# Performance work log

Hardware: AMD Instinct MI355X
Metric: run time of the kernel (lower is better)

Reference implementation:

```python
import jax, jax.numpy as jnp
import numpy as np

HALF = 16  # num_outputs // 2 with num_features = 32
EPS = 1e-5


def _gmul(Wm, h):
    # Wm: [B,N,M,J], h: [B,M,F] -> [B,N,J*F] (j-major feature layout, matching torch split/cat/bmm)
    B, N = Wm.shape[0], Wm.shape[1]
    return jnp.einsum('bnmj,bmf->bnjf', Wm, h).reshape(B, N, -1)


def _bn(z, g, b):
    # training-mode BatchNorm2d on [R, C, 1, 1] == per-channel norm over rows, biased var
    m = z.mean(axis=0)
    v = z.var(axis=0)
    return g * (z - m) / jnp.sqrt(v + EPS) + b


def _block(W, hx, W_lg, hy, P, wx2x, wy2x, bx, wy2y, wx2y, by, gx, btx, gy, bty):
    B, N, M = P.shape[0], P.shape[1], P.shape[2]
    x2x = _gmul(W, hx).reshape(-1, wx2x.shape[0])
    y2x = _gmul(P, hy).reshape(-1, wy2x.shape[0])
    zx = x2x @ wx2x + y2x @ wy2x + bx
    zx = jnp.concatenate([jax.nn.relu(zx[:, :HALF]), zx[:, HALF:]], axis=1)
    xo = _bn(zx, gx, btx).reshape(B, N, -1)
    y2y = _gmul(W_lg, hy).reshape(-1, wy2y.shape[0])
    x2y = _gmul(jnp.swapaxes(P, 1, 2), hx).reshape(-1, wx2y.shape[0])
    zy = y2y @ wy2y + x2y @ wx2y + by
    zy = jnp.concatenate([jax.nn.relu(zy[:, :HALF]), zy[:, HALF:]], axis=1)
    yo = _bn(zy, gy, bty).reshape(B, M, -1)
    return xo, yo


def _forward(W, x, W_lg, y, P,
             wx2x0, wy2x0, bx0, wy2y0, wx2y0, by0, gx0, btx0, gy0, bty0,
             wx2x_m, wy2x_m, bx_m, wy2y_m, wx2y_m, by_m, gx_m, btx_m, gy_m, bty_m,
             wlx, wly, bl):
    hx, hy = _block(W, x, W_lg, y, P, wx2x0, wy2x0, bx0, wy2y0, wx2y0, by0,
                    gx0, btx0, gy0, bty0)
    for i in range(wx2x_m.shape[0]):  # fixed num_layers loop
        hx, hy = _block(W, hx, W_lg, hy, P,
                        wx2x_m[i], wy2x_m[i], bx_m[i], wy2y_m[i], wx2y_m[i], by_m[i],
                        gx_m[i], btx_m[i], gy_m[i], bty_m[i])
    # final layer: linear only, x branch output
    x2x = _gmul(W, hx).reshape(-1, wlx.shape[0])
    y2x = _gmul(P, hy).reshape(-1, wly.shape[0])
    out = (x2x @ wlx + y2x @ wly + bl).reshape(W.shape[0], W.shape[1], -1)
    return out


def setup_inputs() -> dict:
    key = jax.random.key(0)
    ks = iter(jax.random.split(key, 40))
    B, N, M, J, F, L, C = 1, 2048, 4096, 3, 32, 6, 2
    d = {}
    d['W'] = jax.random.normal(next(ks), (B, N, N, J), jnp.float32)
    d['x'] = jax.random.normal(next(ks), (B, N, 1), jnp.float32)
    d['W_lg'] = jax.random.normal(next(ks), (B, M, M, J), jnp.float32)
    d['y'] = jax.random.normal(next(ks), (B, M, 1), jnp.float32)
    d['P'] = jax.random.normal(next(ks), (B, N, M, 2), jnp.float32)
    s = 0.1
    d['wx2x0'] = jax.random.normal(next(ks), (J * 1, F), jnp.float32) * s
    d['wy2x0'] = jax.random.normal(next(ks), (2 * 1, F), jnp.float32) * s
    d['bx0'] = jax.random.normal(next(ks), (F,), jnp.float32) * s
    d['wy2y0'] = jax.random.normal(next(ks), (J * 1, F), jnp.float32) * s
    d['wx2y0'] = jax.random.normal(next(ks), (2 * 1, F), jnp.float32) * s
    d['by0'] = jax.random.normal(next(ks), (F,), jnp.float32) * s
    d['gx0'] = jnp.ones((F,), jnp.float32)
    d['btx0'] = jnp.zeros((F,), jnp.float32)
    d['gy0'] = jnp.ones((F,), jnp.float32)
    d['bty0'] = jnp.zeros((F,), jnp.float32)
    d['wx2x_m'] = jax.random.normal(next(ks), (L, J * F, F), jnp.float32) * s
    d['wy2x_m'] = jax.random.normal(next(ks), (L, 2 * F, F), jnp.float32) * s
    d['bx_m'] = jax.random.normal(next(ks), (L, F), jnp.float32) * s
    d['wy2y_m'] = jax.random.normal(next(ks), (L, J * F, F), jnp.float32) * s
    d['wx2y_m'] = jax.random.normal(next(ks), (L, 2 * F, F), jnp.float32) * s
    d['by_m'] = jax.random.normal(next(ks), (L, F), jnp.float32) * s
    d['gx_m'] = jnp.ones((L, F), jnp.float32)
    d['btx_m'] = jnp.zeros((L, F), jnp.float32)
    d['gy_m'] = jnp.ones((L, F), jnp.float32)
    d['bty_m'] = jnp.zeros((L, F), jnp.float32)
    d['wlx'] = jax.random.normal(next(ks), (J * F, C), jnp.float32) * s
    d['wly'] = jax.random.normal(next(ks), (2 * F, C), jnp.float32) * s
    d['bl'] = jax.random.normal(next(ks), (C,), jnp.float32) * s
    return d


def reference(W, x, W_lg, y, P,
              wx2x0, wy2x0, bx0, wy2y0, wx2y0, by0, gx0, btx0, gy0, bty0,
              wx2x_m, wy2x_m, bx_m, wy2y_m, wx2y_m, by_m, gx_m, btx_m, gy_m, bty_m,
              wlx, wly, bl):
    return _forward(W, x, W_lg, y, P,
                    wx2x0, wy2x0, bx0, wy2y0, wx2y0, by0, gx0, btx0, gy0, bty0,
                    wx2x_m, wy2x_m, bx_m, wy2y_m, wx2y_m, by_m, gx_m, btx_m, gy_m, bty_m,
                    wlx, wly, bl)
```

## Files before the change

kernel.cpp:

```cpp
#include <hip/hip_runtime.h>

typedef _Float16 f16x8 __attribute__((ext_vector_type(8)));
typedef float f32x4 __attribute__((ext_vector_type(4)));


__device__ inline unsigned short f16b(float v) {
    _Float16 h = (_Float16)v;
    return __builtin_bit_cast(unsigned short, h);
}

__device__ inline void atomAddF(float* p, float v) {
    __hip_atomic_fetch_add(p, v, __ATOMIC_RELAXED, __HIP_MEMORY_SCOPE_AGENT);
}

template<int K>
__device__ inline void pack_cvt(const float* __restrict__ src, unsigned short* __restrict__ dst, int u) {
    int o = u * 8;
    int panel = o / (K * 16);
    int rem = o - panel * (K * 16);
    int kstep = rem >> 9;
    int rem2 = rem & 511;
    int g = rem2 >> 7;
    int r15 = (rem2 >> 3) & 15;
    int row = (panel << 4) | r15;
    int k = (kstep << 5) | (g << 3);
    const float4* s = (const float4*)(src + (size_t)row * K + k);
    float4 v0 = s[0], v1 = s[1];
    uint4 q;
    q.x = (unsigned)f16b(v0.x) | ((unsigned)f16b(v0.y) << 16);
    q.y = (unsigned)f16b(v0.z) | ((unsigned)f16b(v0.w) << 16);
    q.z = (unsigned)f16b(v1.x) | ((unsigned)f16b(v1.y) << 16);
    q.w = (unsigned)f16b(v1.z) | ((unsigned)f16b(v1.w) << 16);
    ((uint4*)dst)[u] = q;
}

__global__ __launch_bounds__(256) void cvt_pack(const float* __restrict__ W, const float* __restrict__ WL,
                                                unsigned short* __restrict__ Wb, unsigned short* __restrict__ WLb) {
    const int NW = 1572864, TOT = 1572864 + 6291456;
    for (int u = blockIdx.x * 256 + threadIdx.x; u < TOT; u += 2048 * 256) {
        if (u < NW) pack_cvt<6144>(W, Wb, u);
        else pack_cvt<12288>(WL, WLb, u - NW);
    }
}

__global__ __launch_bounds__(256) void transpose_p(const float* __restrict__ P,
                                                   unsigned short* __restrict__ Pb,
                                                   unsigned short* __restrict__ PT) {
    __shared__ unsigned int lds[64][33];
    int bid = blockIdx.x;
    int m0 = (bid & 127) * 32;
    int n0 = (bid >> 7) * 64;
    int tid = threadIdx.x;
    const float2* P2 = (const float2*)P;
    #pragma unroll
    for (int it = 0; it < 8; ++it) {
        int idx = it * 256 + tid;
        int nl = idx >> 5, ml = idx & 31;
        float2 v = P2[(size_t)(n0 + nl) * 4096 + (m0 + ml)];
        unsigned int pk = (unsigned int)f16b(v.x) | ((unsigned int)f16b(v.y) << 16);
        lds[nl][ml] = pk;
    }
    __syncthreads();
    unsigned int* PTu = (unsigned int*)PT;
    #pragma unroll
    for (int it = 0; it < 8; ++it) {
        int idx = it * 256 + tid;
        int ml = idx >> 6, nl = idx & 63;
        int row = m0 + ml;
        int k2 = (n0 + nl) * 2;
        int o = ((row >> 4) << 16) | ((k2 >> 5) << 9) | (((((k2 >> 3) & 3) << 4) | (row & 15)) << 3) | (k2 & 7);
        PTu[o >> 1] = lds[nl][ml];
    }
    unsigned int* Pbu = (unsigned int*)Pb;
    #pragma unroll
    for (int it = 0; it < 8; ++it) {
        int idx = it * 256 + tid;
        int nl = idx >> 5, ml = idx & 31;
        int row = n0 + nl;
        int k = (m0 + ml) * 2;
        int o = (row >> 4) * 131072 + ((k >> 5) << 9) + (((((k >> 3) & 3) << 4) | (row & 15)) << 3) + (k & 7);
        Pbu[o >> 1] = lds[nl][ml];
    }
}

__global__ __launch_bounds__(256) void build_b(
    const float* __restrict__ srcx, const float* __restrict__ srcy,
    int Fin, int Fout, int buildB2, int use_bn,
    const float* __restrict__ stats,
    const float* __restrict__ w1a, const float* __restrict__ w1b,
    const float* __restrict__ w2a, const float* __restrict__ w2b,
    unsigned short* __restrict__ B1f, unsigned short* __restrict__ B2f) {
    int tid0 = blockIdx.x * 256 + threadIdx.x;
    const int NB1 = 14336 * 32;
    int isB2 = 0, t2 = tid0;
    if (tid0 >= NB1) {
        if (!buildB2) return;
        isB2 = 1; t2 = tid0 - NB1;
        if (t2 >= 16384 * 32) return;
    }
    int e = t2 & 7, lane = (t2 >> 3) & 63, hh = (t2 >> 9) & 1, t = t2 >> 10;
    int k = (t << 5) | ((lane >> 4) << 3) | e;
    int g = (hh << 4) | (lane & 15);
    float v = 0.f;
    if (g < Fout) {
        const float* hr; const float* wc; int useY;
        if (!isB2) {
            if (k < 6144) { int m = k / 3, j = k - 3 * m; hr = srcx + m * Fin; wc = w1a + (j * Fin) * Fout + g; useY = 0; }
            else { int k2 = k - 6144; int m = k2 >> 1, p = k2 & 1; hr = srcy + m * Fin; wc = w1b + (p * Fin) * Fout + g; useY = 1; }
        } else {
            if (k < 12288) { int m = k / 3, j = k - 3 * m; hr = srcy + m * Fin; wc = w2a + (j * Fin) * Fout + g; useY = 1; }
            else { int k2 = k - 12288; int n = k2 >> 1, p = k2 & 1; hr = srcx + n * Fin; wc = w2b + (p * Fin) * Fout + g; useY = 0; }
        }
        float a = 0.f;
        if (use_bn) {
            const float* sc = useY ? stats + 196 : stats + 132;
            const float* sh = useY ? stats + 228 : stats + 164;
            #pragma unroll
            for (int f = 0; f < 32; ++f) {
                float h = sc[f] * hr[f] + sh[f];
                a += h * wc[f * Fout];
            }
        } else {
            for (int f = 0; f < Fin; ++f) a += hr[f] * wc[f * Fout];
        }
        v = a;
    }
    if (!isB2) B1f[t2] = f16b(v); else B2f[t2] = f16b(v);
}

__global__ __launch_bounds__(256) void gemm_k(
    const unsigned short* __restrict__ Wb, const unsigned short* __restrict__ Pb,
    const unsigned short* __restrict__ WLb, const unsigned short* __restrict__ PTb,
    const unsigned short* __restrict__ B1f, const unsigned short* __restrict__ B2f,
    float* __restrict__ px, float* __restrict__ py, float* __restrict__ stats, int nwgx) {
    __shared__ float lds[4][1024];
    int bid = blockIdx.x;
    if (bid == 0 && threadIdx.x < 132) stats[threadIdx.x] = 0.f;
    const unsigned short* Bf;
    float* Z;
    int seg, Mbase, K, kloc, kb;
    const unsigned short* A16;
    if (bid < nwgx) {
        Bf = B1f;
        int mwg = bid / 14; seg = bid % 14;
        Mbase = mwg * 32;
        kb = seg << 10;
        Z = px + (size_t)seg * 65536;
        if (seg < 6) { K = 6144; kloc = kb;        A16 = Wb; }
        else         { K = 8192; kloc = kb - 6144; A16 = Pb; }
    } else {
        int b2 = bid - nwgx;
        Bf = B2f;
        int mwg = b2 / 16; seg = b2 % 16;
        Mbase = mwg * 32;
        kb = seg << 10;
        Z = py + (size_t)seg * 131072;
        if (seg < 12) { K = 12288; kloc = kb;         A16 = WLb; }
        else          { K = 4096;  kloc = kb - 12288; A16 = PTb; }
    }
    int wid = threadIdx.x >> 6, lane = threadIdx.x & 63;
    int kq = wid << 8;
    const unsigned short* ap0 = A16 + (size_t)(Mbase >> 4) * (K * 16)
                              + (size_t)((kloc + kq) >> 5) * 512 + lane * 8;
    const unsigned short* ap1 = ap0 + (size_t)K * 16;
    const unsigned short* bp = Bf + ((size_t)((kb + kq) >> 5)) * 1024 + lane * 8;
    f32x4 acc00 = {0.f,0.f,0.f,0.f}, acc01 = {0.f,0.f,0.f,0.f};
    f32x4 acc10 = {0.f,0.f,0.f,0.f}, acc11 = {0.f,0.f,0.f,0.f};
    #pragma unroll
    for (int ks = 0; ks < 8; ++ks) {
        f16x8 a0 = *(const f16x8*)ap0;
        f16x8 a1 = *(const f16x8*)ap1;
        f16x8 b0 = *(const f16x8*)bp;
        f16x8 b1 = *(const f16x8*)(bp + 512);
        acc00 = __builtin_amdgcn_mfma_f32_16x16x32_f16(a0, b0, acc00, 0, 0, 0);
        acc10 = __builtin_amdgcn_mfma_f32_16x16x32_f16(a1, b0, acc10, 0, 0, 0);
        acc01 = __builtin_amdgcn_mfma_f32_16x16x32_f16(a0, b1, acc01, 0, 0, 0);
        acc11 = __builtin_amdgcn_mfma_f32_16x16x32_f16(a1, b1, acc11, 0, 0, 0);
        ap0 += 512; ap1 += 512; bp += 1024;
    }
    int col = lane & 15, r0 = (lane >> 4) << 2;
    float* l = lds[wid];
    #pragma unroll
    for (int r = 0; r < 4; ++r) {
        l[(r0 + r) * 32 + col]            = acc00[r];
        l[(r0 + r) * 32 + col + 16]       = acc01[r];
        l[(r0 + r + 16) * 32 + col]       = acc10[r];
        l[(r0 + r + 16) * 32 + col + 16]  = acc11[r];
    }
    __syncthreads();
    int t = threadIdx.x;
    float4 a = ((const float4*)lds[0])[t];
    float4 b = ((const float4*)lds[1])[t];
    float4 c = ((const float4*)lds[2])[t];
    float4 d = ((const float4*)lds[3])[t];
    float4 s;
    s.x = (a.x + b.x) + (c.x + d.x);
    s.y = (a.y + b.y) + (c.y + d.y);
    s.z = (a.z + b.z) + (c.z + d.z);
    s.w = (a.w + b.w) + (c.w + d.w);
    ((float4*)(Z + (size_t)Mbase * 32))[t] = s;
}

__global__ __launch_bounds__(256) void reduce_stats(
    const float* __restrict__ px, const float* __restrict__ py,
    const float* __restrict__ bx, const float* __restrict__ by,
    const float* __restrict__ gx, const float* __restrict__ btx,
    const float* __restrict__ gy, const float* __restrict__ bty,
    float* __restrict__ zax, float* __restrict__ zay,
    float* __restrict__ stats) {
    __shared__ float lsum[4][8][8];
    __shared__ int lastFlag;
    int bid = blockIdx.x, tid = threadIdx.x;
    const float4* src; const float* bias; float4* dst; float* st; int nseg, i4, stride4;
    if (bid < 64) { src = (const float4*)px; bias = bx; dst = (float4*)zax; st = stats;      nseg = 14; i4 = bid * 256 + tid;        stride4 = 16384; }
    else          { src = (const float4*)py; bias = by; dst = (float4*)zay; st = stats + 64; nseg = 16; i4 = (bid - 64) * 256 + tid; stride4 = 32768; }
    float4 s = {0.f, 0.f, 0.f, 0.f};
    for (int g = 0; g < nseg; ++g) {
        float4 v = src[(size_t)g * stride4 + i4];
        s.x += v.x; s.y += v.y; s.z += v.z; s.w += v.w;
    }
    int c0 = (i4 & 7) * 4;
    float4 b4 = *(const float4*)(bias + c0);
    s.x += b4.x; s.y += b4.y; s.z += b4.z; s.w += b4.w;
    if (c0 < 16) {
        s.x = fmaxf(s.x, 0.f); s.y = fmaxf(s.y, 0.f);
        s.z = fmaxf(s.z, 0.f); s.w = fmaxf(s.w, 0.f);
    }
    dst[i4] = s;
    float4 s2 = {s.x * s.x, s.y * s.y, s.z * s.z, s.w * s.w};
    #pragma unroll
    for (int mask = 8; mask <= 32; mask <<= 1) {
        s.x += __shfl_xor(s.x, mask); s.y += __shfl_xor(s.y, mask);
        s.z += __shfl_xor(s.z, mask); s.w += __shfl_xor(s.w, mask);
        s2.x += __shfl_xor(s2.x, mask); s2.y += __shfl_xor(s2.y, mask);
        s2.z += __shfl_xor(s2.z, mask); s2.w += __shfl_xor(s2.w, mask);
    }
    int w = tid >> 6, ln = tid & 63;
    if (ln < 8) {
        lsum[w][ln][0] = s.x;  lsum[w][ln][1] = s.y;  lsum[w][ln][2] = s.z;  lsum[w][ln][3] = s.w;
        lsum[w][ln][4] = s2.x; lsum[w][ln][5] = s2.y; lsum[w][ln][6] = s2.z; lsum[w][ln][7] = s2.w;
    }
    __syncthreads();
    if (tid < 64) {
        int q = tid >> 3, e = tid & 7;
        float v = lsum[0][q][e] + lsum[1][q][e] + lsum[2][q][e] + lsum[3][q][e];
        int col = q * 4 + (e & 3);
        atomAddF((e < 4) ? &st[col] : &st[32 + col], v);
    }
    __syncthreads();
    if (tid == 0) {
        __threadfence();
        int old = __hip_atomic_fetch_add((int*)(stats + 128), 1, __ATOMIC_ACQ_REL, __HIP_MEMORY_SCOPE_AGENT);
        lastFlag = (old == 191) ? 1 : 0;
    }
    __syncthreads();
    if (lastFlag && tid < 64) {
        int f = tid & 31, isY = tid >> 5;
        float* sb = stats + (isY ? 64 : 0);
        float n = isY ? 4096.f : 2048.f;
        float sum = __hip_atomic_load(&sb[f], __ATOMIC_RELAXED, __HIP_MEMORY_SCOPE_AGENT);
        float ssq = __hip_atomic_load(&sb[32 + f], __ATOMIC_RELAXED, __HIP_MEMORY_SCOPE_AGENT);
        float mean = sum / n;
        float var = ssq / n - mean * mean;
        const float* gv = isY ? gy : gx;
        const float* bv = isY ? bty : btx;
        float sc = gv[f] * rsqrtf(var + 1e-5f);
        stats[132 + isY * 64 + f] = sc;
        stats[164 + isY * 64 + f] = bv[f] - mean * sc;
    }
}

__global__ __launch_bounds__(256) void out_final(const float* __restrict__ px,
                                                 const float* __restrict__ bl,
                                                 float* __restrict__ out) {
    int tid = blockIdx.x * 256 + threadIdx.x;
    if (tid < 4096) {
        int n = tid >> 1, c = tid & 1;
        float a = bl[c];
        for (int s = 0; s < 14; ++s) a += px[(size_t)s * 65536 + n * 32 + c];
        out[tid] = a;
    }
}

extern "C" void kernel_launch(void* const* d_in, const int* in_sizes, int n_in,
                              void* d_out, int out_size, void* d_ws, size_t ws_size,
                              hipStream_t stream) {
    const float* W    = (const float*)d_in[0];
    const float* x    = (const float*)d_in[1];
    const float* WL   = (const float*)d_in[2];
    const float* y    = (const float*)d_in[3];
    const float* P    = (const float*)d_in[4];
    const float* wx2x0 = (const float*)d_in[5];
    const float* wy2x0 = (const float*)d_in[6];
    const float* bx0   = (const float*)d_in[7];
    const float* wy2y0 = (const float*)d_in[8];
    const float* wx2y0 = (const float*)d_in[9];
    const float* by0   = (const float*)d_in[10];
    const float* gx0   = (const float*)d_in[11];
    const float* btx0  = (const float*)d_in[12];
    const float* gy0   = (const float*)d_in[13];
    const float* bty0  = (const float*)d_in[14];
    const float* wx2x_m = (const float*)d_in[15];
    const float* wy2x_m = (const float*)d_in[16];
    const float* bx_m   = (const float*)d_in[17];
    const float* wy2y_m = (const float*)d_in[18];
    const float* wx2y_m = (const float*)d_in[19];
    const float* by_m   = (const float*)d_in[20];
    const float* gx_m   = (const float*)d_in[21];
    const float* btx_m  = (const float*)d_in[22];
    const float* gy_m   = (const float*)d_in[23];
    const float* bty_m  = (const float*)d_in[24];
    const float* wlx = (const float*)d_in[25];
    const float* wly = (const float*)d_in[26];
    const float* bl  = (const float*)d_in[27];

    char* base = (char*)d_ws;
    unsigned short* Wb  = (unsigned short*)(base + 0);
    unsigned short* Pb  = (unsigned short*)(base + 25165824);
    unsigned short* WLb = (unsigned short*)(base + 58720256);
    unsigned short* PTb = (unsigned short*)(base + 159383552);
    unsigned short* B1f = (unsigned short*)(base + 192937984);
    unsigned short* B2f = (unsigned short*)(base + 193855488);
    float* zax   = (float*)(base + 194904064);
    float* zay   = (float*)(base + 195166208);
    float* stats = (float*)(base + 195690496);
    float* px    = (float*)(base + 195692544);
    float* py    = (float*)(base + 199362560);

    cvt_pack<<<2048, 256, 0, stream>>>(W, WL, Wb, WLb);
    transpose_p<<<4096, 256, 0, stream>>>(P, Pb, PTb);

    build_b<<<3840, 256, 0, stream>>>(x, y, 1, 32, 1, 0, stats,
                                      wx2x0, wy2x0, wy2y0, wx2y0, B1f, B2f);
    gemm_k<<<2944, 256, 0, stream>>>(Wb, Pb, WLb, PTb, B1f, B2f, px, py, stats, 896);
    reduce_stats<<<192, 256, 0, stream>>>(px, py, bx0, by0, gx0, btx0, gy0, bty0, zax, zay, stats);

    for (int i = 0; i < 6; ++i) {
        build_b<<<3840, 256, 0, stream>>>(zax, zay, 32, 32, 1, 1, stats,
                                          wx2x_m + i * 3072, wy2x_m + i * 2048,
                                          wy2y_m + i * 3072, wx2y_m + i * 2048, B1f, B2f);
        gemm_k<<<2944, 256, 0, stream>>>(Wb, Pb, WLb, PTb, B1f, B2f, px, py, stats, 896);
        reduce_stats<<<192, 256, 0, stream>>>(px, py, bx_m + i * 32, by_m + i * 32,
                                              gx_m + i * 32, btx_m + i * 32,
                                              gy_m + i * 32, bty_m + i * 32, zax, zay, stats);
    }

    build_b<<<1792, 256, 0, stream>>>(zax, zay, 32, 2, 0, 1, stats,
                                      wlx, wly, nullptr, nullptr, B1f, B2f);
    gemm_k<<<896, 256, 0, stream>>>(Wb, Pb, WLb, PTb, B1f, B2f, px, py, stats, 896);
    out_final<<<16, 256, 0, stream>>>(px, bl, (float*)d_out);
}
```

Baseline: 679.7 us.

## Merge pack and transpose into one prep kernel; coalesce conversion reads

Fuses the fp16 pack/convert of W and W_lg with the P transpose into a single launch, with block ranges split between the two jobs. Each pack thread now reads a contiguous 32-float run of one row instead of 8 floats, and scatters four 16-byte stores. build_b is remapped so that adjacent threads share a k and differ in output column g, which makes the input-row reads broadcast-friendly while the stores become scattered. The intent is to cut launch overhead and improve read coalescing, at the cost of less regular writes.

```diff
diff --git a/kernel.cpp b/kernel.cpp
--- a/kernel.cpp
+++ b/kernel.cpp
@@ -14,42 +14,44 @@
 }
 
 template<int K>
-__device__ inline void pack_cvt(const float* __restrict__ src, unsigned short* __restrict__ dst, int u) {
-    int o = u * 8;
-    int panel = o / (K * 16);
-    int rem = o - panel * (K * 16);
-    int kstep = rem >> 9;
-    int rem2 = rem & 511;
-    int g = rem2 >> 7;
-    int r15 = (rem2 >> 3) & 15;
+__device__ inline void pack_cvt4(const float* __restrict__ src, unsigned short* __restrict__ dst, int q) {
+    const int KSTEPS = K / 32;
+    int r15 = q & 15;
+    int blk = q >> 4;
+    int panel = blk / KSTEPS;
+    int kstep = blk - panel * KSTEPS;
     int row = (panel << 4) | r15;
-    int k = (kstep << 5) | (g << 3);
-    const float4* s = (const float4*)(src + (size_t)row * K + k);
-    float4 v0 = s[0], v1 = s[1];
-    uint4 q;
-    q.x = (unsigned)f16b(v0.x) | ((unsigned)f16b(v0.y) << 16);
-    q.y = (unsigned)f16b(v0.z) | ((unsigned)f16b(v0.w) << 16);
-    q.z = (unsigned)f16b(v1.x) | ((unsigned)f16b(v1.y) << 16);
-    q.w = (unsigned)f16b(v1.z) | ((unsigned)f16b(v1.w) << 16);
-    ((uint4*)dst)[u] = q;
-}
-
-__global__ __launch_bounds__(256) void cvt_pack(const float* __restrict__ W, const float* __restrict__ WL,
-                                                unsigned short* __restrict__ Wb, unsigned short* __restrict__ WLb) {
-    const int NW = 1572864, TOT = 1572864 + 6291456;
-    for (int u = blockIdx.x * 256 + threadIdx.x; u < TOT; u += 2048 * 256) {
-        if (u < NW) pack_cvt<6144>(W, Wb, u);
-        else pack_cvt<12288>(WL, WLb, u - NW);
-    }
-}
-
-__global__ __launch_bounds__(256) void transpose_p(const float* __restrict__ P,
-                                                   unsigned short* __restrict__ Pb,
-                                                   unsigned short* __restrict__ PT) {
+    const float4* s = (const float4*)(src + (size_t)row * K + (kstep << 5));
+    uint4* d = (uint4*)dst;
+    #pragma unroll
+    for (int g = 0; g < 4; ++g) {
+        float4 v0 = s[g * 2], v1 = s[g * 2 + 1];
+        uint4 qq;
+        qq.x = (unsigned)f16b(v0.x) | ((unsigned)f16b(v0.y) << 16);
+        qq.y = (unsigned)f16b(v0.z) | ((unsigned)f16b(v0.w) << 16);
+        qq.z = (unsigned)f16b(v1.x) | ((unsigned)f16b(v1.y) << 16);
+        qq.w = (unsigned)f16b(v1.z) | ((unsigned)f16b(v1.w) << 16);
+        d[(size_t)blk * 64 + g * 16 + r15] = qq;
+    }
+}
+
+__global__ __launch_bounds__(256) void prep(const float* __restrict__ W, const float* __restrict__ WL,
+                                            const float* __restrict__ P,
+                                            unsigned short* __restrict__ Wb, unsigned short* __restrict__ WLb,
+                                            unsigned short* __restrict__ Pb, unsigned short* __restrict__ PT) {
     __shared__ unsigned int lds[64][33];
     int bid = blockIdx.x;
-    int m0 = (bid & 127) * 32;
-    int n0 = (bid >> 7) * 64;
+    if (bid < 2048) {
+        const int QW = 393216, QTOT = 393216 + 1572864;
+        for (int q = bid * 256 + threadIdx.x; q < QTOT; q += 2048 * 256) {
+            if (q < QW) pack_cvt4<6144>(W, Wb, q);
+            else pack_cvt4<12288>(WL, WLb, q - QW);
+        }
+        return;
+    }
+    int vb = bid - 2048;
+    int m0 = (vb & 127) * 32;
+    int n0 = (vb >> 7) * 64;
     int tid = threadIdx.x;
     const float2* P2 = (const float2*)P;
     #pragma unroll
@@ -90,17 +92,16 @@
     const float* __restrict__ w1a, const float* __restrict__ w1b,
     const float* __restrict__ w2a, const float* __restrict__ w2b,
     unsigned short* __restrict__ B1f, unsigned short* __restrict__ B2f) {
-    int tid0 = blockIdx.x * 256 + threadIdx.x;
+    int t2 = blockIdx.x * 256 + threadIdx.x;
     const int NB1 = 14336 * 32;
-    int isB2 = 0, t2 = tid0;
-    if (tid0 >= NB1) {
+    int isB2 = 0;
+    if (t2 >= NB1) {
         if (!buildB2) return;
-        isB2 = 1; t2 = tid0 - NB1;
+        isB2 = 1; t2 -= NB1;
         if (t2 >= 16384 * 32) return;
     }
-    int e = t2 & 7, lane = (t2 >> 3) & 63, hh = (t2 >> 9) & 1, t = t2 >> 10;
-    int k = (t << 5) | ((lane >> 4) << 3) | e;
-    int g = (hh << 4) | (lane & 15);
+    int g = t2 & 31;
+    int k = t2 >> 5;
     float v = 0.f;
     if (g < Fout) {
         const float* hr; const float* wc; int useY;
@@ -125,7 +126,9 @@
         }
         v = a;
     }
-    if (!isB2) B1f[t2] = f16b(v); else B2f[t2] = f16b(v);
+    int e = k & 7, kw = (k >> 3) & 3, t = k >> 5, hh = g >> 4;
+    int off = (((t * 2 + hh) * 64 + (kw << 4) + (g & 15)) << 3) | e;
+    if (!isB2) B1f[off] = f16b(v); else B2f[off] = f16b(v);
 }
 
 __global__ __launch_bounds__(256) void gemm_k(
@@ -327,8 +330,7 @@
     float* px    = (float*)(base + 195692544);
     float* py    = (float*)(base + 199362560);
 
-    cvt_pack<<<2048, 256, 0, stream>>>(W, WL, Wb, WLb);
-    transpose_p<<<4096, 256, 0, stream>>>(P, Pb, PTb);
+    prep<<<6144, 256, 0, stream>>>(W, WL, P, Wb, WLb, Pb, PTb);
 
     build_b<<<3840, 256, 0, stream>>>(x, y, 1, 32, 1, 0, stats,
                                       wx2x0, wy2x0, wy2y0, wx2y0, B1f, B2f);
```

Result: faster. 618.3 us (-9.0%).
